# Kernel tuning notes

Hardware: AMD Instinct MI355X
Metric: run time of the kernel (lower is better)

## Reference

```python
import jax, jax.numpy as jnp
import numpy as np

B, S, E, H = 2, 4096, 512, 8
D = E // H  # head_dim = 64


def setup_inputs() -> dict:
    key = jax.random.key(0)
    ks = jax.random.split(key, 5)
    s = E ** -0.5
    return {
        "x": jax.random.normal(ks[0], (B, S, E), dtype=jnp.float32),
        "w_qkv": jax.random.normal(ks[1], (E, 3 * E), dtype=jnp.float32) * s,
        "b_qkv": jnp.zeros((3 * E,), dtype=jnp.float32),
        "w_out": jax.random.normal(ks[2], (E, E), dtype=jnp.float32) * s,
        "b_out": jnp.zeros((E,), dtype=jnp.float32),
    }


def reference(x, w_qkv, b_qkv, w_out, b_out):
    # qkv projection: [B,S,3E] -> [3,B,H,S,D]
    qkv = (x @ w_qkv + b_qkv).reshape(B, S, 3, H, D).transpose(2, 0, 3, 1, 4)
    q, k, v = qkv[0], qkv[1], qkv[2]
    # full score matrix [B,H,S,S] (faithful to the unfused torch impl)
    attn = jnp.einsum("bhqd,bhkd->bhqk", q, k) * (D ** -0.5)
    attn = jax.nn.softmax(attn, axis=-1)
    # dropout in eval mode -> identity (deterministic reference)
    out = jnp.einsum("bhqk,bhkd->bhqd", attn, v)  # [B,H,S,D]
    out = out.transpose(0, 2, 1, 3).reshape(B, S, E)
    return out @ w_out + b_out
```

## Files before the change

### kernel.cpp

```cpp
#include <hip/hip_runtime.h>

typedef __attribute__((ext_vector_type(8))) short bf16x8;
typedef __attribute__((ext_vector_type(4))) float f32x4;

#define MFMA16 __builtin_amdgcn_mfma_f32_16x16x32_bf16

__device__ __forceinline__ unsigned short f2bf(float f) {
  unsigned int u = __builtin_bit_cast(unsigned int, f);
  u += 0x7FFFu + ((u >> 16) & 1u);
  return (unsigned short)(u >> 16);
}

__device__ __forceinline__ void load_lds16(const void* g, void* l) {
  __builtin_amdgcn_global_load_lds(
      (const __attribute__((address_space(1))) unsigned int*)g,
      (__attribute__((address_space(3))) unsigned int*)l, 16, 0, 0);
}

__global__ __launch_bounds__(256) void prep_kernel(
    const float* __restrict__ x, const float* __restrict__ wqkv,
    const float* __restrict__ wout, unsigned short* __restrict__ xb,
    unsigned short* __restrict__ wqkvT, unsigned short* __restrict__ woutT) {
  int blk = blockIdx.x;
  int t = threadIdx.x;
  if (blk < 4096) {
    int i = (blk * 256 + t) * 4;
    float4 v = *(const float4*)(x + i);
    ushort4 o;
    o.x = f2bf(v.x); o.y = f2bf(v.y); o.z = f2bf(v.z); o.w = f2bf(v.w);
    *(ushort4*)(xb + i) = o;
  } else if (blk < 4864) {
    int u = ((blk - 4096) * 256 + t) * 4;
    int k = u / 1536, n = u % 1536;
    float4 v = *(const float4*)(wqkv + (size_t)k * 1536 + n);
    wqkvT[(size_t)(n + 0) * 512 + k] = f2bf(v.x);
    wqkvT[(size_t)(n + 1) * 512 + k] = f2bf(v.y);
    wqkvT[(size_t)(n + 2) * 512 + k] = f2bf(v.z);
    wqkvT[(size_t)(n + 3) * 512 + k] = f2bf(v.w);
  } else {
    int u = ((blk - 4864) * 256 + t) * 4;
    int k = u >> 9, n = u & 511;
    float4 v = *(const float4*)(wout + (size_t)k * 512 + n);
    woutT[(size_t)(n + 0) * 512 + k] = f2bf(v.x);
    woutT[(size_t)(n + 1) * 512 + k] = f2bf(v.y);
    woutT[(size_t)(n + 2) * 512 + k] = f2bf(v.z);
    woutT[(size_t)(n + 3) * 512 + k] = f2bf(v.w);
  }
}

__global__ __launch_bounds__(256, 2) void qkv_gemm(
    const unsigned short* __restrict__ xb, const unsigned short* __restrict__ bt,
    const float* __restrict__ bias, unsigned short* __restrict__ qout,
    unsigned short* __restrict__ ksw, unsigned short* __restrict__ vtsw) {
  __shared__ unsigned short As[128 * 32];
  __shared__ unsigned short Bs[128 * 32];
  const int t = threadIdx.x;
  const int lane = t & 63;
  const int llo = lane & 15, lhi = lane >> 4;
  const int w = t >> 6, wr = w >> 1, wc = w & 1;
  const int m0 = blockIdx.x * 128, n0 = blockIdx.y * 128;

  f32x4 acc[4][4];
#pragma unroll
  for (int i = 0; i < 4; ++i)
#pragma unroll
    for (int j = 0; j < 4; ++j) acc[i][j] = (f32x4){0.f, 0.f, 0.f, 0.f};

  const int r0 = t >> 2;
  const int sb = (t & 3) * 16;

  for (int k0 = 0; k0 < 512; k0 += 32) {
    const char* ga = (const char*)xb + (size_t)(m0 + r0) * 1024 + k0 * 2 + sb;
    const char* gb = (const char*)bt + (size_t)(n0 + r0) * 1024 + k0 * 2 + sb;
    load_lds16(ga, (char*)As + t * 16);
    load_lds16(ga + 64 * 1024, (char*)As + 4096 + t * 16);
    load_lds16(gb, (char*)Bs + t * 16);
    load_lds16(gb + 64 * 1024, (char*)Bs + 4096 + t * 16);
    __syncthreads();

    bf16x8 af[4], bf[4];
#pragma unroll
    for (int mi = 0; mi < 4; ++mi)
      af[mi] = *(const bf16x8*)(As + (wr * 64 + mi * 16 + llo) * 32 + lhi * 8);
#pragma unroll
    for (int ni = 0; ni < 4; ++ni)
      bf[ni] = *(const bf16x8*)(Bs + (wc * 64 + ni * 16 + llo) * 32 + lhi * 8);
#pragma unroll
    for (int mi = 0; mi < 4; ++mi)
#pragma unroll
      for (int ni = 0; ni < 4; ++ni)
        acc[mi][ni] = MFMA16(af[mi], bf[ni], acc[mi][ni], 0, 0, 0);
    __syncthreads();
  }

#pragma unroll
  for (int ni = 0; ni < 4; ++ni) {
    int col = n0 + wc * 64 + ni * 16 + llo;
    float bv = bias[col];
    int sec = col >> 9;
    int h = (col >> 6) & 7;
    int d = col & 63;
#pragma unroll
    for (int mi = 0; mi < 4; ++mi) {
      int rowb = m0 + wr * 64 + mi * 16 + lhi * 4;
#pragma unroll
      for (int r = 0; r < 4; ++r) {
        int m = rowb + r;
        int b = m >> 12, s = m & 4095;
        int bh = (b << 3) + h;
        float val = acc[mi][ni][r] + bv;
        if (sec == 0) {
          qout[((size_t)bh * 4096 + s) * 64 + d] = f2bf(val * 0.18033688f);
        } else if (sec == 1) {
          size_t byte = (size_t)bh * 524288 + (size_t)(s >> 6) * 8192 +
                        (size_t)(s & 63) * 128 + ((d * 2) ^ ((s & 7) << 4));
          *(unsigned short*)((char*)ksw + byte) = f2bf(val);
        } else {
          int u64k = s & 63;
          int c = u64k >> 4, u = u64k & 15;
          int kperm = ((c >> 1) << 5) + ((u >> 2) << 3) + ((c & 1) << 2) + (u & 3);
          size_t byte = (size_t)bh * 524288 + (size_t)(s >> 6) * 8192 +
                        (size_t)d * 128 + ((kperm * 2) ^ ((d & 7) << 4));
          *(unsigned short*)((char*)vtsw + byte) = f2bf(val);
        }
      }
    }
  }
}

__global__ __launch_bounds__(256, 2) void attn_kernel(
    const unsigned short* __restrict__ qp, const unsigned short* __restrict__ ksw,
    const unsigned short* __restrict__ vtsw, unsigned short* __restrict__ aout) {
  __shared__ unsigned short Ks[2][4096];
  __shared__ unsigned short Vts[2][4096];

  const int t = threadIdx.x, lane = t & 63, w = t >> 6;
  const int llo = lane & 15, lhi = lane >> 4;

  const int wg = blockIdx.x + (blockIdx.y << 5);
  const int pidx = ((wg & 7) << 6) + (wg >> 3);
  const int bh = pidx >> 5;
  const int q0 = (pidx & 31) * 128 + w * 32;

  bf16x8 qf[2][2];
#pragma unroll
  for (int qs = 0; qs < 2; ++qs)
#pragma unroll
    for (int f = 0; f < 2; ++f) {
      int row = q0 + qs * 16 + llo;
      int d = f * 32 + lhi * 8;
      qf[qs][f] = *(const bf16x8*)(qp + ((size_t)bh * 4096 + row) * 64 + d);
    }

  float lpart[2] = {0.f, 0.f};
  f32x4 o[2][4];
#pragma unroll
  for (int qs = 0; qs < 2; ++qs)
#pragma unroll
    for (int di = 0; di < 4; ++di) o[qs][di] = (f32x4){0.f, 0.f, 0.f, 0.f};

  const char* kbase = (const char*)ksw + (size_t)bh * 524288;
  const char* vbase = (const char*)vtsw + (size_t)bh * 524288;

  load_lds16(kbase + t * 16, (char*)&Ks[0][0] + t * 16);
  load_lds16(kbase + 4096 + t * 16, (char*)&Ks[0][0] + 4096 + t * 16);
  load_lds16(vbase + t * 16, (char*)&Vts[0][0] + t * 16);
  load_lds16(vbase + 4096 + t * 16, (char*)&Vts[0][0] + 4096 + t * 16);
  __syncthreads();

  int cur = 0;
  for (int kt = 0; kt < 64; ++kt) {
    if (kt + 1 < 64) {
      const char* kn = kbase + (kt + 1) * 8192;
      const char* vn = vbase + (kt + 1) * 8192;
      char* kd = (char*)&Ks[cur ^ 1][0];
      char* vd = (char*)&Vts[cur ^ 1][0];
      load_lds16(kn + t * 16, kd + t * 16);
      load_lds16(kn + 4096 + t * 16, kd + 4096 + t * 16);
      load_lds16(vn + t * 16, vd + t * 16);
      load_lds16(vn + 4096 + t * 16, vd + 4096 + t * 16);
    }
    const char* kcur = (const char*)&Ks[cur][0];
    const char* vcur = (const char*)&Vts[cur][0];

    f32x4 sc[2][4];
#pragma unroll
    for (int c = 0; c < 4; ++c) {
      int krow = c * 16 + llo;
      int sw = (krow & 7) << 4;
      bf16x8 kf0 = *(const bf16x8*)(kcur + krow * 128 + ((lhi * 16) ^ sw));
      bf16x8 kf1 = *(const bf16x8*)(kcur + krow * 128 + ((lhi * 16 + 64) ^ sw));
#pragma unroll
      for (int qs = 0; qs < 2; ++qs) {
        sc[qs][c] = MFMA16(kf0, qf[qs][0], (f32x4){0.f, 0.f, 0.f, 0.f}, 0, 0, 0);
        sc[qs][c] = MFMA16(kf1, qf[qs][1], sc[qs][c], 0, 0, 0);
      }
    }

    bf16x8 pf[2][2];
#pragma unroll
    for (int qs = 0; qs < 2; ++qs) {
      float e[4][4];
#pragma unroll
      for (int c = 0; c < 4; ++c)
#pragma unroll
        for (int r = 0; r < 4; ++r) {
          e[c][r] = __builtin_amdgcn_exp2f(sc[qs][c][r]);
          lpart[qs] += e[c][r];
        }
#pragma unroll
      for (int f = 0; f < 2; ++f) {
        bf16x8 pv;
#pragma unroll
        for (int j = 0; j < 8; ++j)
          pv[j] = (short)f2bf(e[2 * f + (j >> 2)][j & 3]);
        pf[qs][f] = pv;
      }
    }

#pragma unroll
    for (int f = 0; f < 2; ++f) {
#pragma unroll
      for (int di = 0; di < 4; ++di) {
        int vrow = di * 16 + llo;
        int byte = vrow * 128 + ((lhi * 16 + f * 64) ^ ((vrow & 7) << 4));
        bf16x8 vf = *(const bf16x8*)(vcur + byte);
#pragma unroll
        for (int qs = 0; qs < 2; ++qs)
          o[qs][di] = MFMA16(pf[qs][f], vf, o[qs][di], 0, 0, 0);
      }
    }
    __syncthreads();
    cur ^= 1;
  }

  float linv[2][4];
#pragma unroll
  for (int qs = 0; qs < 2; ++qs) {
    float s = lpart[qs];
    s += __shfl_xor(s, 16, 64);
    s += __shfl_xor(s, 32, 64);
#pragma unroll
    for (int r = 0; r < 4; ++r)
      linv[qs][r] = 1.f / __shfl(s, lhi * 4 + r, 64);
  }

  int b = bh >> 3, h = bh & 7;
#pragma unroll
  for (int qs = 0; qs < 2; ++qs)
#pragma unroll
    for (int di = 0; di < 4; ++di)
#pragma unroll
      for (int r = 0; r < 4; ++r) {
        int s = q0 + qs * 16 + lhi * 4 + r;
        int d = di * 16 + llo;
        float val = o[qs][di][r] * linv[qs][r];
        aout[((size_t)b * 4096 + s) * 512 + h * 64 + d] = f2bf(val);
      }
}

__global__ __launch_bounds__(256, 2) void out_gemm(
    const unsigned short* __restrict__ ab, const unsigned short* __restrict__ bt,
    const float* __restrict__ bias, float* __restrict__ out) {
  __shared__ unsigned short As[128 * 32];
  __shared__ unsigned short Bs[128 * 32];
  const int t = threadIdx.x;
  const int lane = t & 63;
  const int llo = lane & 15, lhi = lane >> 4;
  const int w = t >> 6, wr = w >> 1, wc = w & 1;
  const int m0 = blockIdx.x * 128, n0 = blockIdx.y * 128;

  f32x4 acc[4][4];
#pragma unroll
  for (int i = 0; i < 4; ++i)
#pragma unroll
    for (int j = 0; j < 4; ++j) acc[i][j] = (f32x4){0.f, 0.f, 0.f, 0.f};

  const int r0 = t >> 2;
  const int sb = (t & 3) * 16;

  for (int k0 = 0; k0 < 512; k0 += 32) {
    const char* ga = (const char*)ab + (size_t)(m0 + r0) * 1024 + k0 * 2 + sb;
    const char* gb = (const char*)bt + (size_t)(n0 + r0) * 1024 + k0 * 2 + sb;
    load_lds16(ga, (char*)As + t * 16);
    load_lds16(ga + 64 * 1024, (char*)As + 4096 + t * 16);
    load_lds16(gb, (char*)Bs + t * 16);
    load_lds16(gb + 64 * 1024, (char*)Bs + 4096 + t * 16);
    __syncthreads();

    bf16x8 af[4], bf[4];
#pragma unroll
    for (int mi = 0; mi < 4; ++mi)
      af[mi] = *(const bf16x8*)(As + (wr * 64 + mi * 16 + llo) * 32 + lhi * 8);
#pragma unroll
    for (int ni = 0; ni < 4; ++ni)
      bf[ni] = *(const bf16x8*)(Bs + (wc * 64 + ni * 16 + llo) * 32 + lhi * 8);
#pragma unroll
    for (int mi = 0; mi < 4; ++mi)
#pragma unroll
      for (int ni = 0; ni < 4; ++ni)
        acc[mi][ni] = MFMA16(af[mi], bf[ni], acc[mi][ni], 0, 0, 0);
    __syncthreads();
  }

#pragma unroll
  for (int ni = 0; ni < 4; ++ni) {
    int col = n0 + wc * 64 + ni * 16 + llo;
    float bv = bias[col];
#pragma unroll
    for (int mi = 0; mi < 4; ++mi) {
      int rowb = m0 + wr * 64 + mi * 16 + lhi * 4;
#pragma unroll
      for (int r = 0; r < 4; ++r)
        out[(size_t)(rowb + r) * 512 + col] = acc[mi][ni][r] + bv;
    }
  }
}

extern "C" void kernel_launch(void* const* d_in, const int* in_sizes, int n_in,
                              void* d_out, int out_size, void* d_ws, size_t ws_size,
                              hipStream_t stream) {
  const float* x = (const float*)d_in[0];
  const float* wqkv = (const float*)d_in[1];
  const float* bqkv = (const float*)d_in[2];
  const float* wout = (const float*)d_in[3];
  const float* bout = (const float*)d_in[4];
  float* out = (float*)d_out;

  char* ws = (char*)d_ws;
  unsigned short* xb    = (unsigned short*)(ws + 0);
  unsigned short* wqkvT = (unsigned short*)(ws + 8388608);
  unsigned short* woutT = (unsigned short*)(ws + 9961472);
  unsigned short* qb    = (unsigned short*)(ws + 10485760);
  unsigned short* ksw   = (unsigned short*)(ws + 18874368);
  unsigned short* vtsw  = (unsigned short*)(ws + 27262976);
  unsigned short* ab    = (unsigned short*)(ws + 35651584);
  (void)ws_size; (void)in_sizes; (void)n_in; (void)out_size;

  prep_kernel<<<5120, 256, 0, stream>>>(x, wqkv, wout, xb, wqkvT, woutT);
  qkv_gemm<<<dim3(64, 12), 256, 0, stream>>>(xb, wqkvT, bqkv, qb, ksw, vtsw);
  attn_kernel<<<dim3(32, 16), 256, 0, stream>>>(qb, ksw, vtsw, ab);
  out_gemm<<<dim3(64, 4), 256, 0, stream>>>(ab, woutT, bout, out);
}
```

Before: 146.5 us.

## Software-pipeline QK^T of the next tile with softmax and PV of the current tile

```diff
diff --git a/kernel.cpp b/kernel.cpp
--- a/kernel.cpp
+++ b/kernel.cpp
@@ -1,4 +1,5 @@
 #include <hip/hip_runtime.h>
+#include <hip/hip_bf16.h>
 
 typedef __attribute__((ext_vector_type(8))) short bf16x8;
 typedef __attribute__((ext_vector_type(4))) float f32x4;
@@ -162,42 +163,31 @@
   const char* kbase = (const char*)ksw + (size_t)bh * 524288;
   const char* vbase = (const char*)vtsw + (size_t)bh * 524288;
 
-  load_lds16(kbase + t * 16, (char*)&Ks[0][0] + t * 16);
-  load_lds16(kbase + 4096 + t * 16, (char*)&Ks[0][0] + 4096 + t * 16);
-  load_lds16(vbase + t * 16, (char*)&Vts[0][0] + t * 16);
-  load_lds16(vbase + 4096 + t * 16, (char*)&Vts[0][0] + 4096 + t * 16);
-  __syncthreads();
-
-  int cur = 0;
-  for (int kt = 0; kt < 64; ++kt) {
-    if (kt + 1 < 64) {
-      const char* kn = kbase + (kt + 1) * 8192;
-      const char* vn = vbase + (kt + 1) * 8192;
-      char* kd = (char*)&Ks[cur ^ 1][0];
-      char* vd = (char*)&Vts[cur ^ 1][0];
-      load_lds16(kn + t * 16, kd + t * 16);
-      load_lds16(kn + 4096 + t * 16, kd + 4096 + t * 16);
-      load_lds16(vn + t * 16, vd + t * 16);
-      load_lds16(vn + 4096 + t * 16, vd + 4096 + t * 16);
-    }
-    const char* kcur = (const char*)&Ks[cur][0];
-    const char* vcur = (const char*)&Vts[cur][0];
-
-    f32x4 sc[2][4];
+  bf16x8 pf[2][2];
+
+  auto stage_tile = [&](const char* g, char* d) {
+    load_lds16(g + t * 16, d + t * 16);
+    load_lds16(g + 4096 + t * 16, d + 4096 + t * 16);
+  };
+
+  auto qkt = [&](f32x4 (&sc)[2][4], const char* kbuf) {
+    __builtin_amdgcn_s_setprio(1);
 #pragma unroll
     for (int c = 0; c < 4; ++c) {
       int krow = c * 16 + llo;
       int sw = (krow & 7) << 4;
-      bf16x8 kf0 = *(const bf16x8*)(kcur + krow * 128 + ((lhi * 16) ^ sw));
-      bf16x8 kf1 = *(const bf16x8*)(kcur + krow * 128 + ((lhi * 16 + 64) ^ sw));
+      bf16x8 kf0 = *(const bf16x8*)(kbuf + krow * 128 + ((lhi * 16) ^ sw));
+      bf16x8 kf1 = *(const bf16x8*)(kbuf + krow * 128 + ((lhi * 16 + 64) ^ sw));
 #pragma unroll
       for (int qs = 0; qs < 2; ++qs) {
         sc[qs][c] = MFMA16(kf0, qf[qs][0], (f32x4){0.f, 0.f, 0.f, 0.f}, 0, 0, 0);
         sc[qs][c] = MFMA16(kf1, qf[qs][1], sc[qs][c], 0, 0, 0);
       }
     }
-
-    bf16x8 pf[2][2];
+    __builtin_amdgcn_s_setprio(0);
+  };
+
+  auto softmax_pack = [&](f32x4 (&sc)[2][4]) {
 #pragma unroll
     for (int qs = 0; qs < 2; ++qs) {
       float e[4][4];
@@ -210,29 +200,63 @@
         }
 #pragma unroll
       for (int f = 0; f < 2; ++f) {
-        bf16x8 pv;
+        bf16x8 pvv;
 #pragma unroll
         for (int j = 0; j < 8; ++j)
-          pv[j] = (short)f2bf(e[2 * f + (j >> 2)][j & 3]);
-        pf[qs][f] = pv;
-      }
-    }
-
-#pragma unroll
-    for (int f = 0; f < 2; ++f) {
+          pvv[j] = __builtin_bit_cast(short,
+                       __float2bfloat16(e[2 * f + (j >> 2)][j & 3]));
+        pf[qs][f] = pvv;
+      }
+    }
+  };
+
+  auto pv_accum = [&](const char* vbuf) {
+    __builtin_amdgcn_s_setprio(1);
+#pragma unroll
+    for (int f = 0; f < 2; ++f)
 #pragma unroll
       for (int di = 0; di < 4; ++di) {
         int vrow = di * 16 + llo;
         int byte = vrow * 128 + ((lhi * 16 + f * 64) ^ ((vrow & 7) << 4));
-        bf16x8 vf = *(const bf16x8*)(vcur + byte);
+        bf16x8 vf = *(const bf16x8*)(vbuf + byte);
 #pragma unroll
         for (int qs = 0; qs < 2; ++qs)
           o[qs][di] = MFMA16(pf[qs][f], vf, o[qs][di], 0, 0, 0);
       }
-    }
-    __syncthreads();
-    cur ^= 1;
-  }
+    __builtin_amdgcn_s_setprio(0);
+  };
+
+  stage_tile(kbase, (char*)&Ks[0][0]);
+  stage_tile(vbase, (char*)&Vts[0][0]);
+  stage_tile(kbase + 8192, (char*)&Ks[1][0]);
+  __syncthreads();
+
+  f32x4 scA[2][4], scB[2][4];
+  qkt(scA, (const char*)&Ks[0][0]);
+  __syncthreads();
+
+  for (int kt = 0; kt < 62; kt += 2) {
+    stage_tile(kbase + (size_t)(kt + 2) * 8192, (char*)&Ks[0][0]);
+    stage_tile(vbase + (size_t)(kt + 1) * 8192, (char*)&Vts[1][0]);
+    qkt(scB, (const char*)&Ks[1][0]);
+    softmax_pack(scA);
+    pv_accum((const char*)&Vts[0][0]);
+    __syncthreads();
+    stage_tile(kbase + (size_t)(kt + 3) * 8192, (char*)&Ks[1][0]);
+    stage_tile(vbase + (size_t)(kt + 2) * 8192, (char*)&Vts[0][0]);
+    qkt(scA, (const char*)&Ks[0][0]);
+    softmax_pack(scB);
+    pv_accum((const char*)&Vts[1][0]);
+    __syncthreads();
+  }
+
+  stage_tile(vbase + (size_t)63 * 8192, (char*)&Vts[1][0]);
+  qkt(scB, (const char*)&Ks[1][0]);
+  softmax_pack(scA);
+  pv_accum((const char*)&Vts[0][0]);
+  __syncthreads();
+  softmax_pack(scB);
+  pv_accum((const char*)&Vts[1][0]);
 
   float linv[2][4];
 #pragma unroll
```

After: 132.2 us. 1.11x faster.
